# Kernel tuning notes

Hardware: AMD Instinct MI355X
Metric: run time of the kernel (lower is better)

The kernel has to match this reference:

```python
import jax, jax.numpy as jnp
import numpy as np

D = 768      # embed_dim
L = 8        # depth
NH = 4       # num_heads
HD = D // NH # head_dim = 192
GS = 16      # grid size (max_grid_size)
S = GS * GS  # 256 tokens
B = 64
EPS = 1.1920929e-07  # torch.finfo(float32).eps (RMSNorm eps=None)


def rmsnorm(x):
    return x * jax.lax.rsqrt(jnp.mean(x * x, axis=-1, keepdims=True) + EPS)


def householder_Q(vs):
    # sequential chain of Householder reflections: Q <- Q - (2/||v||^2) v (v^T Q)
    def step(Q, v):
        v = v[:, None]
        Q = Q - (2.0 / (jnp.sum(v * v) + 1e-08)) * (v @ (v.T @ Q))
        return Q, None
    Q, _ = jax.lax.scan(step, jnp.eye(vs.shape[1], dtype=vs.dtype), vs)
    return Q


def setup_inputs() -> dict:
    key = jax.random.key(0)
    ks = jax.random.split(key, 16)
    r = lambda k, shape, s=0.02: jax.random.normal(k, shape, jnp.float32) * s
    return dict(
        z_t=jax.random.normal(ks[0], (B, 3, 32, 32), jnp.float32),
        logsnr=jax.random.normal(ks[1], (B,), jnp.float32),
        qkv_w=r(ks[2], (L, D, 3 * D)),
        out_w=r(ks[3], (L, D, D)),
        gate_w=r(ks[4], (L, D, D)), gate_b=jnp.zeros((L, D), jnp.float32),
        mlpg_w=r(ks[5], (L, D, 8 * D)), mlpg_b=jnp.zeros((L, 8 * D), jnp.float32),
        mlpo_w=r(ks[6], (L, 4 * D, D)), mlpo_b=jnp.zeros((L, D), jnp.float32),
        hh_vs=r(ks[7], (L, HD // 2, HD)),
        patch_w=r(ks[8], (20, D)), patch_b=jnp.zeros((D,), jnp.float32),
        head_w=r(ks[9], (D, 12)), head_b=jnp.zeros((12,), jnp.float32),
        sd1_w=r(ks[10], (8, D)), sd1_b=jnp.zeros((D,), jnp.float32),
        sd2_w=r(ks[11], (D, 12)), sd2_b=jnp.zeros((12,), jnp.float32),
        lam_w=r(ks[12], (D, 1)), lam_b=jnp.zeros((1,), jnp.float32),
    )


def reference(z_t, logsnr, qkv_w, out_w, gate_w, gate_b, mlpg_w, mlpg_b,
              mlpo_w, mlpo_b, hh_vs, patch_w, patch_b, head_w, head_b,
              sd1_w, sd1_b, sd2_w, sd2_b, lam_w, lam_b):
    Bn, C, Him, Wim = z_t.shape
    gh = Him // 2
    # patchify 2x2 -> [B, S, 12]
    patches = z_t.reshape(Bn, C, gh, 2, gh, 2).transpose(0, 2, 4, 1, 3, 5).reshape(Bn, S, 12)
    # FourierFeatures(num_bands=4) -> 8-dim sin/cos embedding of logsnr
    bands = 2.0 ** jnp.arange(4, dtype=jnp.float32)
    ang = logsnr[:, None] * bands
    spins = jnp.concatenate([jnp.sin(ang), jnp.cos(ang)], axis=-1)  # [B, 8]
    x = jnp.concatenate([patches, jnp.broadcast_to(spins[:, None, :], (Bn, S, 8))], axis=-1) @ patch_w + patch_b

    # 2D RoPE tables on the 16x16 grid
    yy, xx = jnp.meshgrid(jnp.arange(GS), jnp.arange(GS), indexing='ij')
    coords = jnp.stack([yy.ravel(), xx.ravel()], axis=1).astype(jnp.float32)  # [S, 2]
    dim_half = HD // 2
    inv_freq = 1.0 / 10000.0 ** (jnp.arange(0, dim_half, 2, dtype=jnp.float32) / dim_half)
    fy = coords[:, 0:1] * inv_freq
    fx = coords[:, 1:2] * inv_freq
    emb = jnp.concatenate([fy, fx, fy, fx], axis=-1)  # [S, HD]
    cos, sin = jnp.cos(emb), jnp.sin(emb)

    # local sliding-window mask: euclidean distance on grid < 2.5
    d2 = jnp.sum((coords[:, None, :] - coords[None, :, :]) ** 2, axis=-1)
    local_mask = d2 < 2.5 ** 2  # [S, S]
    is_glob = jnp.array([(i + 1) % 4 == 0 for i in range(L)])
    scale = 1.0 / jnp.sqrt(jnp.float32(HD))

    def layer(x, p):
        qw, ow, gw, gb, mgw, mgb, mow, mob, vs, glob = p
        h = rmsnorm(x)
        q, k, v = jnp.split(h @ qw, 3, axis=-1)
        heads = lambda t: t.reshape(Bn, S, NH, HD).transpose(0, 2, 1, 3)  # [B,H,S,hd]
        q, k, v = heads(q), heads(k), heads(v)
        # RnRoPE: inverse Householder -> rotate -> forward Householder
        Q = householder_Q(vs)
        q, k = q @ Q.T, k @ Q.T
        def rot(t):
            t1, t2 = jnp.split(t, 2, axis=-1)
            return t * cos + jnp.concatenate([-t2, t1], axis=-1) * sin
        q, k = rot(q) @ Q, rot(k) @ Q
        scores = jnp.einsum('bhqd,bhkd->bhqk', q, k) * scale
        keep = local_mask | glob  # global layers attend everywhere
        scores = jnp.where(keep, scores, -1e30)
        attn = jax.nn.softmax(scores, axis=-1) @ v  # [B,H,S,hd]
        attn = attn.transpose(0, 2, 1, 3).reshape(Bn, S, D) @ ow
        gate = jax.nn.sigmoid(attn @ gw + gb)
        x = x + attn * gate
        g, val = jnp.split(rmsnorm(x) @ mgw + mgb, 2, axis=-1)
        x = x + (val * jax.nn.gelu(g, approximate=False)) @ mow + mob
        return x, None

    x, _ = jax.lax.scan(layer, x, (qkv_w, out_w, gate_w, gate_b, mlpg_w, mlpg_b,
                                   mlpo_w, mlpo_b, hh_vs, is_glob))
    x = rmsnorm(x)
    z_pred = x @ head_w + head_b  # [B, S, 12]
    # factorized mode: FourierScaleDecoder scale and lambda head
    scale_f = jnp.exp(jax.nn.silu(spins @ sd1_w + sd1_b) @ sd2_w + sd2_b)  # [B, 12]
    z_pred = z_pred * scale_f[:, None, :]
    l_pred = (jnp.mean(x, axis=1) @ lam_w + lam_b)[:, 0]
    z_img = z_pred.reshape(Bn, gh, gh, 3, 2, 2).transpose(0, 3, 1, 4, 2, 5).reshape(Bn, C, Him, Wim)
    return z_img, l_pred
```

## Files before the change

### kernel.cpp

```cpp
#include <hip/hip_runtime.h>
#include <hip/hip_bf16.h>
#include <math.h>


#define DEV static __device__ __forceinline__

typedef float    f32x4 __attribute__((ext_vector_type(4)));
typedef short    s16x8 __attribute__((ext_vector_type(8)));
typedef unsigned short u16x8 __attribute__((ext_vector_type(8)));
typedef unsigned short u16x4 __attribute__((ext_vector_type(4)));

constexpr int Bb = 64, Ss = 256, Dd = 768, Ll = 8, NHh = 4, HDd = 192;
constexpr int M_TOK = Bb * Ss;
constexpr float EPS_RMS = 1.1920929e-07f;
constexpr float ATT_SCALE = 0.07216878364870322f;
constexpr size_t ARENA_K = (size_t)Bb * NHh * Ss * HDd;

constexpr size_t B_SPINS  = 0;
constexpr size_t B_SCALEF = 2048;
constexpr size_t B_QT     = 5120;
constexpr size_t B_COS    = B_QT + 1179648;
constexpr size_t B_SIN    = B_COS + 196608;
constexpr size_t B_G      = B_SIN + 196608;
constexpr size_t B_T      = B_G + 294912;
constexpr size_t B_AWY    = B_T + 294912;
constexpr size_t B_ROWLAM = B_AWY + 589824;
constexpr size_t B_X      = B_ROWLAM + 65536;
constexpr size_t B_H      = B_X + 50331648;
constexpr size_t B_PROJ   = B_H + 25165824;
constexpr size_t B_WEFFT  = B_PROJ + 25165824;
constexpr size_t B_OUTWT  = B_WEFFT + 28311552;
constexpr size_t B_GATEWT = B_OUTWT + 9437184;
constexpr size_t B_MLPGT  = B_GATEWT + 9437184;
constexpr size_t B_MLPOT  = B_MLPGT + 75497472;
constexpr size_t B_ARENA  = B_MLPOT + 37748736;

DEV float sigmoidf_(float x) { return 1.0f / (1.0f + expf(-x)); }
DEV float geluf_(float g)    { return 0.5f * g * (1.0f + erff(g * 0.7071067811865476f)); }
DEV unsigned short f2bf(float f) {
    union { float f; unsigned u; } a; a.f = f;
    unsigned u = a.u + 0x7fffu + ((a.u >> 16) & 1u);
    return (unsigned short)(u >> 16);
}
DEV float b2f(unsigned short u) {
    union { unsigned u; float f; } a; a.u = ((unsigned)u) << 16; return a.f;
}
DEV void gload16(const void* g, void* l) {
    __builtin_amdgcn_global_load_lds((const __attribute__((address_space(1))) void*)g,
                                     (__attribute__((address_space(3))) void*)l, 16, 0, 0);
}

DEV void xcd_chunk(int gx, int gy, int CX, int& bx, int& by) {
    int id = by * gx + bx;
    int c = id & 7;
    int s = id >> 3;
    int CY = gy >> 3;
    int subsz = CY * CX;
    int bxc = s / subsz;
    int r = s - bxc * subsz;
    int byl = r / CX;
    by = c * CY + byl;
    bx = bxc * CX + (r - byl * CX);
}

__global__ void spins_kernel(const float* __restrict__ logsnr, float* __restrict__ spins) {
    int b = threadIdx.x;
    if (b < 64) {
        float v = logsnr[b];
#pragma unroll
        for (int j = 0; j < 4; ++j) {
            float ang = v * (float)(1 << j);
            spins[b * 8 + j]     = sinf(ang);
            spins[b * 8 + 4 + j] = cosf(ang);
        }
    }
}

__global__ void rope_table_kernel(float* __restrict__ cosb, float* __restrict__ sinb) {
    int s = blockIdx.x, j = threadIdx.x;
    int y = s >> 4, x = s & 15;
    int base = j % 96;
    float coord, invf;
    if (base < 48) { invf = expf(-(float)base * (2.0f / 96.0f) * 9.210340371976184f); coord = (float)y; }
    else { int i = base - 48; invf = expf(-(float)i * (2.0f / 96.0f) * 9.210340371976184f); coord = (float)x; }
    float f = coord * invf, sv, cv;
    sincosf(f, &sv, &cv);
    cosb[s * 192 + j] = cv;
    sinb[s * 192 + j] = sv;
}

__global__ __launch_bounds__(256) void hh_gram_kernel(const float* __restrict__ hh_vs,
                                                      float* __restrict__ Gm) {
    __shared__ float Y[96][192];
    int l = blockIdx.x, t = threadIdx.x;
    const float4* src = (const float4*)(hh_vs + (size_t)l * 96 * 192);
    for (int i = t; i < 4608; i += 256) ((float4*)&Y[0][0])[i] = src[i];
    __syncthreads();
    for (int e = t; e < 9216; e += 256) {
        int i = e / 96, j = e - (e / 96) * 96;
        float acc = 0.f;
        for (int d = 0; d < 48; ++d) {
            float4 a = *(const float4*)&Y[i][d * 4];
            float4 b = *(const float4*)&Y[j][d * 4];
            acc += a.x * b.x + a.y * b.y + a.z * b.z + a.w * b.w;
        }
        Gm[(size_t)l * 9216 + e] = acc;
    }
}

__global__ __launch_bounds__(128) void hh_t_kernel(const float* __restrict__ Gm,
                                                   float* __restrict__ Tm) {
    __shared__ float G[96][96];
    __shared__ float Tt[96][96];
    int l = blockIdx.x, t = threadIdx.x;
    const float* Gl = Gm + (size_t)l * 9216;
    for (int i = t; i < 9216; i += 128) { ((float*)G)[i] = Gl[i]; ((float*)Tt)[i] = 0.f; }
    __syncthreads();
    if (t < 96) Tt[t][t] = 2.0f / (G[t][t] + 1e-8f);
    __syncthreads();
    for (int j = 1; j < 96; ++j) {
        if (t < 96) {
            float cj = 2.0f / (G[j][j] + 1e-8f);
            float dot = 0.f;
            for (int p = 0; p < j; ++p) dot += Tt[p][t] * G[p][j];
            if (t < j) Tt[j][t] = -cj * dot;
        }
        __syncthreads();
    }
    for (int i = t; i < 9216; i += 128) Tm[(size_t)l * 9216 + i] = ((float*)Tt)[i];
}

__global__ __launch_bounds__(256) void hh_a_kernel(const float* __restrict__ Tm,
                                                   const float* __restrict__ hh_vs,
                                                   float* __restrict__ Am) {
    __shared__ float T[96][96];
    __shared__ float Y[96][192];
    int l = blockIdx.x, t = threadIdx.x;
    const float* Tl = Tm + (size_t)l * 9216;
    const float4* src = (const float4*)(hh_vs + (size_t)l * 96 * 192);
    for (int i = t; i < 9216; i += 256) ((float*)T)[i] = Tl[i];
    for (int i = t; i < 4608; i += 256) ((float4*)&Y[0][0])[i] = src[i];
    __syncthreads();
    for (int idx = t; idx < 4608; idx += 256) {
        int i = idx / 48, e0 = (idx % 48) * 4;
        float4 acc = {0.f, 0.f, 0.f, 0.f};
        for (int j = i; j < 96; ++j) {
            float tv = T[j][i];
            float4 y = *(const float4*)&Y[j][e0];
            acc.x += tv * y.x; acc.y += tv * y.y; acc.z += tv * y.z; acc.w += tv * y.w;
        }
        *(float4*)(Am + (size_t)l * 96 * 192 + (size_t)i * 192 + e0) = acc;
    }
}

__global__ __launch_bounds__(256) void hh_p_kernel(const float* __restrict__ hh_vs,
                                                   const float* __restrict__ Am,
                                                   float* __restrict__ qt) {
    __shared__ float Y[96][192];
    __shared__ float A[96][192];
    int l = blockIdx.x, t = threadIdx.x;
    const float4* ys = (const float4*)(hh_vs + (size_t)l * 96 * 192);
    const float4* as = (const float4*)(Am + (size_t)l * 96 * 192);
    for (int i = t; i < 4608; i += 256) { ((float4*)&Y[0][0])[i] = ys[i]; ((float4*)&A[0][0])[i] = as[i]; }
    __syncthreads();
    for (int idx = t; idx < 9216; idx += 256) {
        int d = idx / 48, e0 = (idx % 48) * 4;
        float4 acc = {0.f, 0.f, 0.f, 0.f};
        for (int i = 0; i < 96; ++i) {
            float yv = Y[i][d];
            float4 a = *(const float4*)&A[i][e0];
            acc.x += yv * a.x; acc.y += yv * a.y; acc.z += yv * a.z; acc.w += yv * a.w;
        }
        acc.x = (d == e0 + 0 ? 1.f : 0.f) - acc.x;
        acc.y = (d == e0 + 1 ? 1.f : 0.f) - acc.y;
        acc.z = (d == e0 + 2 ? 1.f : 0.f) - acc.z;
        acc.w = (d == e0 + 3 ? 1.f : 0.f) - acc.w;
        *(float4*)(qt + (size_t)l * 192 * 192 + (size_t)d * 192 + e0) = acc;
    }
}

__global__ __launch_bounds__(256) void fold_bf16t(const float* __restrict__ qkv_w,
                                                  const float* __restrict__ qt,
                                                  unsigned short* __restrict__ weff_t) {
    int z = blockIdx.z;
    int l = z >> 3, which = (z >> 2) & 1, head = z & 3;
    const float* A  = qkv_w + (size_t)l * 768 * 2304 + (size_t)which * 768 + head * 192;
    const float* Bq = qt + (size_t)l * 192 * 192;
    unsigned short* C = weff_t + (size_t)l * 2304 * 768 + ((size_t)which * 768 + head * 192) * 768;
    int row0 = blockIdx.y * 64, col0 = blockIdx.x * 64;
    __shared__ float As[64][65];
    __shared__ float Bs[64][65];
    int tid = threadIdx.x, tx = tid & 15, ty = tid >> 4;
    float acc[4][4] = {};
    for (int k0 = 0; k0 < 192; k0 += 64) {
        for (int i = tid; i < 1024; i += 256) {
            int r = i >> 4, kq = i & 15;
            float4 va = *(const float4*)(A + (size_t)(row0 + r) * 2304 + k0 + kq * 4);
            As[kq * 4 + 0][r] = va.x; As[kq * 4 + 1][r] = va.y; As[kq * 4 + 2][r] = va.z; As[kq * 4 + 3][r] = va.w;
        }
        for (int i = tid; i < 1024; i += 256) {
            int r = i >> 4, nq = i & 15;
            float4 vb = *(const float4*)(Bq + (size_t)(k0 + r) * 192 + col0 + nq * 4);
            Bs[r][nq * 4 + 0] = vb.x; Bs[r][nq * 4 + 1] = vb.y; Bs[r][nq * 4 + 2] = vb.z; Bs[r][nq * 4 + 3] = vb.w;
        }
        __syncthreads();
        for (int k = 0; k < 64; ++k) {
            float a[4], bb[4];
#pragma unroll
            for (int m = 0; m < 4; ++m) a[m] = As[k][ty * 4 + m];
#pragma unroll
            for (int n = 0; n < 4; ++n) bb[n] = Bs[k][tx * 4 + n];
#pragma unroll
            for (int m = 0; m < 4; ++m)
#pragma unroll
                for (int n = 0; n < 4; ++n) acc[m][n] = fmaf(a[m], bb[n], acc[m][n]);
        }
        __syncthreads();
    }
    float (*Tr)[65] = (float(*)[65])As;
#pragma unroll
    for (int m = 0; m < 4; ++m)
#pragma unroll
        for (int n = 0; n < 4; ++n) Tr[tx * 4 + n][ty * 4 + m] = acc[m][n];
    __syncthreads();
    int nl = tid >> 2, kc = (tid & 3) * 16;
#pragma unroll
    for (int q4 = 0; q4 < 4; ++q4) {
        u16x4 o;
#pragma unroll
        for (int ii = 0; ii < 4; ++ii) o[ii] = f2bf(Tr[nl][kc + q4 * 4 + ii]);
        *(u16x4*)(C + (size_t)(col0 + nl) * 768 + row0 + kc + q4 * 4) = o;
    }
}

__global__ __launch_bounds__(256) void transpose_bf16_kernel(const float* __restrict__ W,
                                                             int ldw, size_t zsrc,
                                                             unsigned short* __restrict__ Wt,
                                                             int ldwt, size_t zdst) {
    __shared__ float t[32][33];
    const float* Wz = W + (size_t)blockIdx.z * zsrc;
    unsigned short* Wtz = Wt + (size_t)blockIdx.z * zdst;
    int k0 = blockIdx.y * 32, n0 = blockIdx.x * 32;
    int tid = threadIdx.x;
    int tr = tid >> 3, tc = tid & 7;
    float4 v = *(const float4*)(Wz + (size_t)(k0 + tr) * ldw + n0 + tc * 4);
    t[tr][tc * 4 + 0] = v.x; t[tr][tc * 4 + 1] = v.y; t[tr][tc * 4 + 2] = v.z; t[tr][tc * 4 + 3] = v.w;
    __syncthreads();
    u16x4 o;
    o[0] = f2bf(t[tc * 4 + 0][tr]); o[1] = f2bf(t[tc * 4 + 1][tr]);
    o[2] = f2bf(t[tc * 4 + 2][tr]); o[3] = f2bf(t[tc * 4 + 3][tr]);
    *(u16x4*)(Wtz + (size_t)(n0 + tr) * ldwt + k0 + tc * 4) = o;
}

__global__ __launch_bounds__(256) void patch_embed_kernel(const float* __restrict__ z_t,
                                                          const float* __restrict__ spins,
                                                          const float* __restrict__ patch_w,
                                                          const float* __restrict__ patch_b,
                                                          float* __restrict__ x) {
    int bs = blockIdx.x;
    int b = bs >> 8, s = bs & 255;
    int gy = s >> 4, gx = s & 15;
    __shared__ float in20[20];
    int t = threadIdx.x;
    if (t < 12) {
        int c = t >> 2, py = (t >> 1) & 1, px = t & 1;
        in20[t] = z_t[(((size_t)b * 3 + c) * 32 + (2 * gy + py)) * 32 + (2 * gx + px)];
    } else if (t < 20) {
        in20[t] = spins[b * 8 + (t - 12)];
    }
    __syncthreads();
    for (int d = t; d < 768; d += 256) {
        float acc = patch_b[d];
#pragma unroll
        for (int i = 0; i < 20; ++i) acc += in20[i] * patch_w[i * 768 + d];
        x[(size_t)bs * 768 + d] = acc;
    }
}

__global__ __launch_bounds__(256) void rmsnorm_kernel(const float* __restrict__ x,
                                                      unsigned short* __restrict__ h) {
    int wave = threadIdx.x >> 6, lane = threadIdx.x & 63;
    int row = blockIdx.x * 4 + wave;
    const float* xr = x + (size_t)row * 768 + lane * 12;
    float4 a = *(const float4*)(xr);
    float4 b = *(const float4*)(xr + 4);
    float4 c = *(const float4*)(xr + 8);
    float ss = a.x*a.x + a.y*a.y + a.z*a.z + a.w*a.w
             + b.x*b.x + b.y*b.y + b.z*b.z + b.w*b.w
             + c.x*c.x + c.y*c.y + c.z*c.z + c.w*c.w;
#pragma unroll
    for (int msk = 1; msk < 64; msk <<= 1) ss += __shfl_xor(ss, msk);
    float sc = 1.0f / sqrtf(ss / 768.0f + EPS_RMS);
    unsigned short* hr = h + (size_t)row * 768 + lane * 12;
    u16x4 o0, o1, o2;
    o0[0]=f2bf(a.x*sc); o0[1]=f2bf(a.y*sc); o0[2]=f2bf(a.z*sc); o0[3]=f2bf(a.w*sc);
    o1[0]=f2bf(b.x*sc); o1[1]=f2bf(b.y*sc); o1[2]=f2bf(b.z*sc); o1[3]=f2bf(b.w*sc);
    o2[0]=f2bf(c.x*sc); o2[1]=f2bf(c.y*sc); o2[2]=f2bf(c.z*sc); o2[3]=f2bf(c.w*sc);
    *(u16x4*)(hr) = o0; *(u16x4*)(hr + 4) = o1; *(u16x4*)(hr + 8) = o2;
}

template <int EPI>
__global__ __launch_bounds__(256) void gemm_mfma(const unsigned short* __restrict__ A, int lda,
                                                 const unsigned short* __restrict__ Bt, int ldb,
                                                 unsigned short* __restrict__ Cb, int ldc, int K,
                                                 const float* __restrict__ bias,
                                                 float* __restrict__ Xf,
                                                 const unsigned short* __restrict__ Pb,
                                                 int CX) {
    __shared__ unsigned short As[2][4096];
    __shared__ unsigned short Bs[2][4096];
    int tid = threadIdx.x;
    int wave = tid >> 6, lane = tid & 63;
    int bx = blockIdx.x, by = blockIdx.y;
    xcd_chunk(gridDim.x, gridDim.y, CX, bx, by);
    int row0 = by * 128, col0 = bx * 128;
    int wm = wave >> 1, wn = wave & 1;
    f32x4 acc[4][4] = {};

    int srow = lane >> 2;
    int ksw = (((lane & 3) ^ (srow & 3)) * 8);
    int lrow = lane & 15;
    int csw = (((lane >> 4) ^ (lane & 3)) * 8);

    auto stage = [&](int buf, int k0) {
#pragma unroll
        for (int it = 0; it < 2; ++it) {
            int chunk = it * 4 + wave;
            int r = chunk * 16 + srow;
            gload16(A  + (size_t)(row0 + r) * lda + k0 + ksw, &As[buf][chunk * 512]);
            gload16(Bt + (size_t)(col0 + r) * ldb + k0 + ksw, &Bs[buf][chunk * 512]);
        }
    };

    int NT = K >> 5;
    stage(0, 0);
    for (int t = 0; t < NT; ++t) {
        if (t + 1 < NT) {
            stage((t + 1) & 1, (t + 1) << 5);
            asm volatile("s_waitcnt vmcnt(4)" ::: "memory");
        } else {
            asm volatile("s_waitcnt vmcnt(0)" ::: "memory");
        }
        __builtin_amdgcn_s_barrier();
        const unsigned short* Ab = As[t & 1];
        const unsigned short* Bb = Bs[t & 1];
        s16x8 af[4], bf[4];
#pragma unroll
        for (int m = 0; m < 4; ++m)
            af[m] = *(const s16x8*)&Ab[(wm * 64 + m * 16 + lrow) * 32 + csw];
#pragma unroll
        for (int n = 0; n < 4; ++n)
            bf[n] = *(const s16x8*)&Bb[(wn * 64 + n * 16 + lrow) * 32 + csw];
#pragma unroll
        for (int m = 0; m < 4; ++m)
#pragma unroll
            for (int n = 0; n < 4; ++n)
                acc[m][n] = __builtin_amdgcn_mfma_f32_16x16x32_bf16(af[m], bf[n], acc[m][n], 0, 0, 0);
        __builtin_amdgcn_s_barrier();
    }

    int lquad = lane >> 4;
#pragma unroll
    for (int m = 0; m < 4; ++m) {
#pragma unroll
        for (int n = 0; n < 4; ++n) {
#pragma unroll
            for (int r = 0; r < 4; ++r) {
                int i = row0 + wm * 64 + m * 16 + lquad * 4 + r;
                int j = col0 + wn * 64 + n * 16 + lrow;
                float v = acc[m][n][r];
                if (bias) v += bias[j];
                if constexpr (EPI == 0) {
                    Cb[(size_t)i * ldc + j] = f2bf(v);
                } else if constexpr (EPI == 1) {
                    int which = j / 768;
                    int rem = j - which * 768;
                    int head = rem / 192;
                    int hd = rem - head * 192;
                    int b = i >> 8, s = i & 255;
                    if (which == 2) {
                        Cb[2 * ARENA_K + (((size_t)(b * 4 + head)) * 192 + hd) * 256 + s] = f2bf(v);
                    } else {
                        Cb[(size_t)which * ARENA_K + (((size_t)(b * 4 + head)) * 256 + s) * 192 + hd] = f2bf(v);
                    }
                } else if constexpr (EPI == 2) {
                    float p = b2f(Pb[(size_t)i * 768 + j]);
                    Xf[(size_t)i * 768 + j] += p * sigmoidf_(v);
                } else if constexpr (EPI == 4) {
                    Xf[(size_t)i * ldc + j] += v;
                }
            }
        }
    }
}

__global__ __launch_bounds__(512) void gemm_mlp_fused(const unsigned short* __restrict__ A,
                                                      const unsigned short* __restrict__ Bt,
                                                      unsigned short* __restrict__ Hid,
                                                      const float* __restrict__ bias,
                                                      int CX) {
    __shared__ unsigned short As[8192];
    __shared__ unsigned short Bs[8192];
    int tid = threadIdx.x;
    int wave = tid >> 6, lane = tid & 63;
    int bx = blockIdx.x, by = blockIdx.y;
    xcd_chunk(gridDim.x, gridDim.y, CX, bx, by);
    int row0 = by * 256, col0 = bx * 64;
    int wm = wave >> 1, wn = wave & 1;
    f32x4 accg[4][2] = {};
    f32x4 accv[4][2] = {};

    int srow = lane >> 2;
    int ksw = (((lane & 3) ^ (srow & 3)) * 8);
    int lrow = lane & 15;
    int csw = (((lane >> 4) ^ (lane & 3)) * 8);

    const unsigned short* Bg = Bt + (size_t)col0 * 768;
    const unsigned short* Bv = Bt + (size_t)(3072 + col0) * 768;

    for (int k0 = 0; k0 < 768; k0 += 32) {
#pragma unroll
        for (int it = 0; it < 2; ++it) {
            int chunk = it * 8 + wave;
            int r = chunk * 16 + srow;
            gload16(A + (size_t)(row0 + r) * 768 + k0 + ksw, &As[chunk * 512]);
        }
        {
            int half = wave >> 2;
            int chunk = wave & 3;
            int r = chunk * 16 + srow;
            const unsigned short* Bh = half ? Bv : Bg;
            gload16(Bh + (size_t)r * 768 + k0 + ksw, &Bs[half * 4096 + chunk * 512]);
        }
        __syncthreads();
        s16x8 af[4], bgf[2], bvf[2];
#pragma unroll
        for (int m = 0; m < 4; ++m)
            af[m] = *(const s16x8*)&As[(wm * 64 + m * 16 + lrow) * 32 + csw];
#pragma unroll
        for (int n = 0; n < 2; ++n) {
            bgf[n] = *(const s16x8*)&Bs[(wn * 32 + n * 16 + lrow) * 32 + csw];
            bvf[n] = *(const s16x8*)&Bs[4096 + (wn * 32 + n * 16 + lrow) * 32 + csw];
        }
#pragma unroll
        for (int m = 0; m < 4; ++m)
#pragma unroll
            for (int n = 0; n < 2; ++n) {
                accg[m][n] = __builtin_amdgcn_mfma_f32_16x16x32_bf16(af[m], bgf[n], accg[m][n], 0, 0, 0);
                accv[m][n] = __builtin_amdgcn_mfma_f32_16x16x32_bf16(af[m], bvf[n], accv[m][n], 0, 0, 0);
            }
        __syncthreads();
    }

    int lquad = lane >> 4;
#pragma unroll
    for (int m = 0; m < 4; ++m) {
#pragma unroll
        for (int n = 0; n < 2; ++n) {
#pragma unroll
            for (int r = 0; r < 4; ++r) {
                int i = row0 + wm * 64 + m * 16 + lquad * 4 + r;
                int j = col0 + wn * 32 + n * 16 + lrow;
                float g = accg[m][n][r] + bias[j];
                float v = accv[m][n][r] + bias[3072 + j];
                Hid[(size_t)i * 3072 + j] = f2bf(v * geluf_(g));
            }
        }
    }
}

__global__ __launch_bounds__(512) void attn_mfma_kernel(const unsigned short* __restrict__ qb_,
                                                        const unsigned short* __restrict__ kb_,
                                                        const unsigned short* __restrict__ vtb_,
                                                        unsigned short* __restrict__ attnb,
                                                        const float* __restrict__ cosb,
                                                        const float* __restrict__ sinb,
                                                        int glob) {
    __shared__ unsigned short Klds[256 * 200];
    __shared__ unsigned short Vlds[192 * 72];
    __shared__ unsigned short Plds[8 * 16 * 72];
    int b = blockIdx.z, hh = blockIdx.y;
    int tid = threadIdx.x;
    int wave = tid >> 6, lane = tid & 63;
    int q0 = blockIdx.x * 128 + wave * 16;
    int yq = q0 >> 4;
    size_t bh = (size_t)(b * 4 + hh);
    const unsigned short* qb  = qb_  + bh * 49152;
    const unsigned short* kb  = kb_  + bh * 49152;
    const unsigned short* vtb = vtb_ + bh * 49152;

    for (int c = tid; c < 6144; c += 512) {
        int r = c / 24, col = c - (c / 24) * 24;
        int j0 = col * 8;
        int jp = j0 < 96 ? j0 + 96 : j0 - 96;
        float sgn = j0 < 96 ? -1.f : 1.f;
        u16x8 a = *(const u16x8*)(kb + (size_t)r * 192 + j0);
        u16x8 p = *(const u16x8*)(kb + (size_t)r * 192 + jp);
        const float* cr = cosb + r * 192 + j0;
        const float* sr = sinb + r * 192 + j0;
        u16x8 o;
#pragma unroll
        for (int i = 0; i < 8; ++i)
            o[i] = f2bf(b2f(a[i]) * cr[i] + sgn * b2f(p[i]) * sr[i]);
        *(u16x8*)&Klds[r * 200 + j0] = o;
    }
    __syncthreads();

    s16x8 qf[6];
    {
        int sq = q0 + (lane & 15);
        const unsigned short* qrow = qb + (size_t)sq * 192;
        const float* cr = cosb + sq * 192;
        const float* sr = sinb + sq * 192;
#pragma unroll
        for (int kk = 0; kk < 6; ++kk) {
            int ck = kk * 32 + (lane >> 4) * 8;
            int cp = ck < 96 ? ck + 96 : ck - 96;
            float sgn = ck < 96 ? -1.f : 1.f;
            u16x8 a = *(const u16x8*)(qrow + ck);
            u16x8 p = *(const u16x8*)(qrow + cp);
            s16x8 o;
#pragma unroll
            for (int i = 0; i < 8; ++i)
                o[i] = (short)f2bf(b2f(a[i]) * cr[ck + i] + sgn * b2f(p[i]) * sr[ck + i]);
            qf[kk] = o;
        }
    }

    f32x4 sc[16];
#pragma unroll
    for (int n = 0; n < 16; ++n) sc[n] = (f32x4){0.f, 0.f, 0.f, 0.f};
#pragma unroll
    for (int kk = 0; kk < 6; ++kk) {
#pragma unroll
        for (int n = 0; n < 16; ++n) {
            if (glob || (n >= yq - 2 && n <= yq + 2)) {
                s16x8 bf = *(const s16x8*)&Klds[(n * 16 + (lane & 15)) * 200 + kk * 32 + (lane >> 4) * 8];
                sc[n] = __builtin_amdgcn_mfma_f32_16x16x32_bf16(qf[kk], bf, sc[n], 0, 0, 0);
            }
        }
    }

    int lq = (lane >> 4) * 4;
#pragma unroll
    for (int n = 0; n < 16; ++n) {
        int sk = n * 16 + (lane & 15);
        int yk = sk >> 4, xk = sk & 15;
#pragma unroll
        for (int r = 0; r < 4; ++r) {
            int sq = q0 + lq + r;
            int dy = (sq >> 4) - yk, dx = (sq & 15) - xk;
            bool keep = glob || (dy * dy + dx * dx) < 7;
            sc[n][r] = keep ? sc[n][r] * ATT_SCALE : -1e30f;
        }
    }
    float rmax[4], rsum[4];
#pragma unroll
    for (int r = 0; r < 4; ++r) {
        float m = sc[0][r];
#pragma unroll
        for (int n = 1; n < 16; ++n) m = fmaxf(m, sc[n][r]);
#pragma unroll
        for (int msk = 1; msk < 16; msk <<= 1) m = fmaxf(m, __shfl_xor(m, msk));
        rmax[r] = m;
    }
#pragma unroll
    for (int r = 0; r < 4; ++r) {
        float e = 0.f;
#pragma unroll
        for (int n = 0; n < 16; ++n) { float p = expf(sc[n][r] - rmax[r]); sc[n][r] = p; e += p; }
#pragma unroll
        for (int msk = 1; msk < 16; msk <<= 1) e += __shfl_xor(e, msk);
        rsum[r] = 1.0f / e;
    }

    f32x4 o[12];
#pragma unroll
    for (int n = 0; n < 12; ++n) o[n] = (f32x4){0.f, 0.f, 0.f, 0.f};
    unsigned short* Pw = &Plds[wave * 1152];
    int ylo = blockIdx.x * 8 - 2, yhi = blockIdx.x * 8 + 9;
    for (int kt = 0; kt < 4; ++kt) {
        if (!glob && !((4 * kt + 3 >= ylo) && (4 * kt <= yhi))) continue;
#pragma unroll
        for (int nn = 0; nn < 4; ++nn) {
#pragma unroll
            for (int r = 0; r < 4; ++r)
                Pw[(lq + r) * 72 + nn * 16 + (lane & 15)] = f2bf(sc[kt * 4 + nn][r] * rsum[r]);
        }
        __syncthreads();
        for (int c = tid; c < 1536; c += 512) {
            int r = c >> 3, col = c & 7;
            *(u16x8*)&Vlds[r * 72 + col * 8] = *(const u16x8*)(vtb + (size_t)r * 256 + kt * 64 + col * 8);
        }
        __syncthreads();
        s16x8 af[2];
#pragma unroll
        for (int kk2 = 0; kk2 < 2; ++kk2)
            af[kk2] = *(const s16x8*)&Pw[(lane & 15) * 72 + kk2 * 32 + (lane >> 4) * 8];
#pragma unroll
        for (int n = 0; n < 12; ++n) {
#pragma unroll
            for (int kk2 = 0; kk2 < 2; ++kk2) {
                s16x8 bf = *(const s16x8*)&Vlds[(n * 16 + (lane & 15)) * 72 + kk2 * 32 + (lane >> 4) * 8];
                o[n] = __builtin_amdgcn_mfma_f32_16x16x32_bf16(af[kk2], bf, o[n], 0, 0, 0);
            }
        }
    }
#pragma unroll
    for (int n = 0; n < 12; ++n) {
        int d = n * 16 + (lane & 15);
#pragma unroll
        for (int r = 0; r < 4; ++r) {
            int sq = q0 + lq + r;
            attnb[((size_t)(b * 256 + sq)) * 768 + hh * 192 + d] = f2bf(o[n][r]);
        }
    }
}

__global__ __launch_bounds__(768) void scalef_kernel(const float* __restrict__ spins,
                                                     const float* __restrict__ sd1_w,
                                                     const float* __restrict__ sd1_b,
                                                     const float* __restrict__ sd2_w,
                                                     const float* __restrict__ sd2_b,
                                                     float* __restrict__ scalef) {
    int b = blockIdx.x, t = threadIdx.x;
    __shared__ float hid[768];
    __shared__ float sp[8];
    if (t < 8) sp[t] = spins[b * 8 + t];
    __syncthreads();
    float acc = sd1_b[t];
#pragma unroll
    for (int i = 0; i < 8; ++i) acc += sp[i] * sd1_w[i * 768 + t];
    hid[t] = acc * sigmoidf_(acc);
    __syncthreads();
    if (t < 12) {
        float o = sd2_b[t];
        for (int d = 0; d < 768; ++d) o += hid[d] * sd2_w[d * 12 + t];
        scalef[b * 12 + t] = expf(o);
    }
}

__global__ __launch_bounds__(256) void head_kernel(const unsigned short* __restrict__ xn,
                                                   const float* __restrict__ head_w,
                                                   const float* __restrict__ head_b,
                                                   const float* __restrict__ scalef,
                                                   const float* __restrict__ lam_w,
                                                   float* __restrict__ out,
                                                   float* __restrict__ rowlam) {
    __shared__ float hw[768][13];
    __shared__ float red[4][64][14];
    int t = threadIdx.x, wave = t >> 6, lane = t & 63;
    for (int i = t; i < 768 * 12; i += 256) hw[i / 12][i % 12] = head_w[i];
    for (int i = t; i < 768; i += 256) hw[i][12] = lam_w[i];
    __syncthreads();
    int row_base = blockIdx.x * 64;
    for (int rr = wave; rr < 64; rr += 4) {
        int row = row_base + rr;
        const unsigned short* xr = xn + (size_t)row * 768 + lane * 12;
        float xv[12];
        u16x4 v0 = *(const u16x4*)(xr);
        u16x4 v1 = *(const u16x4*)(xr + 4);
        u16x4 v2 = *(const u16x4*)(xr + 8);
#pragma unroll
        for (int j = 0; j < 4; ++j) { xv[j] = b2f(v0[j]); xv[4 + j] = b2f(v1[j]); xv[8 + j] = b2f(v2[j]); }
        float p[13] = {};
        int d0 = lane * 12;
#pragma unroll
        for (int dd = 0; dd < 12; ++dd) {
            float xvv = xv[dd];
#pragma unroll
            for (int o = 0; o < 12; ++o) p[o] += xvv * hw[d0 + dd][o];
            p[12] += xvv * hw[d0 + dd][12];
        }
#pragma unroll
        for (int o = 0; o < 13; ++o) red[wave][lane][o] = p[o];
        __syncthreads();
        if (lane < 13) {
            float s = 0.f;
            for (int i = 0; i < 64; ++i) s += red[wave][i][lane];
            if (lane < 12) {
                int b = row >> 8, sidx = row & 255;
                float v = (s + head_b[lane]) * scalef[b * 12 + lane];
                int c = lane >> 2, py = (lane >> 1) & 1, px = lane & 1;
                int gy = sidx >> 4, gxx = sidx & 15;
                out[(((size_t)b * 3 + c) * 32 + 2 * gy + py) * 32 + 2 * gxx + px] = v;
            } else {
                rowlam[row] = s;
            }
        }
        __syncthreads();
    }
}

__global__ __launch_bounds__(256) void lpred_kernel(const float* __restrict__ rowlam,
                                                    const float* __restrict__ lam_b,
                                                    float* __restrict__ out) {
    int b = blockIdx.x, t = threadIdx.x;
    __shared__ float red[256];
    red[t] = rowlam[b * 256 + t];
    __syncthreads();
    for (int s2 = 128; s2 > 0; s2 >>= 1) { if (t < s2) red[t] += red[t + s2]; __syncthreads(); }
    if (t == 0) out[196608 + b] = red[0] / 256.0f + lam_b[0];
}

extern "C" void kernel_launch(void* const* d_in, const int* in_sizes, int n_in,
                              void* d_out, int out_size, void* d_ws, size_t ws_size,
                              hipStream_t stream) {
    const float* z_t     = (const float*)d_in[0];
    const float* logsnr  = (const float*)d_in[1];
    const float* qkv_w   = (const float*)d_in[2];
    const float* out_w   = (const float*)d_in[3];
    const float* gate_w  = (const float*)d_in[4];
    const float* gate_b  = (const float*)d_in[5];
    const float* mlpg_w  = (const float*)d_in[6];
    const float* mlpg_b  = (const float*)d_in[7];
    const float* mlpo_w  = (const float*)d_in[8];
    const float* mlpo_b  = (const float*)d_in[9];
    const float* hh_vs   = (const float*)d_in[10];
    const float* patch_w = (const float*)d_in[11];
    const float* patch_b = (const float*)d_in[12];
    const float* head_w  = (const float*)d_in[13];
    const float* head_b  = (const float*)d_in[14];
    const float* sd1_w   = (const float*)d_in[15];
    const float* sd1_b   = (const float*)d_in[16];
    const float* sd2_w   = (const float*)d_in[17];
    const float* sd2_b   = (const float*)d_in[18];
    const float* lam_w   = (const float*)d_in[19];
    const float* lam_b   = (const float*)d_in[20];

    char* wsb = (char*)d_ws;
    float* spins  = (float*)(wsb + B_SPINS);
    float* scalef = (float*)(wsb + B_SCALEF);
    float* qt     = (float*)(wsb + B_QT);
    float* cosb   = (float*)(wsb + B_COS);
    float* sinb   = (float*)(wsb + B_SIN);
    float* Gm     = (float*)(wsb + B_G);
    float* Tm     = (float*)(wsb + B_T);
    float* Am     = (float*)(wsb + B_AWY);
    float* rowlam = (float*)(wsb + B_ROWLAM);
    float* x      = (float*)(wsb + B_X);
    unsigned short* h      = (unsigned short*)(wsb + B_H);
    unsigned short* proj   = (unsigned short*)(wsb + B_PROJ);
    unsigned short* weff_t = (unsigned short*)(wsb + B_WEFFT);
    unsigned short* outw_t = (unsigned short*)(wsb + B_OUTWT);
    unsigned short* gatew_t= (unsigned short*)(wsb + B_GATEWT);
    unsigned short* mlpg_t = (unsigned short*)(wsb + B_MLPGT);
    unsigned short* mlpo_t = (unsigned short*)(wsb + B_MLPOT);
    unsigned short* arena  = (unsigned short*)(wsb + B_ARENA);
    unsigned short* qbuf = arena;
    unsigned short* kbuf = arena + ARENA_K;
    unsigned short* vtbuf = arena + 2 * ARENA_K;
    unsigned short* attnb = arena + 3 * ARENA_K;
    unsigned short* hidden = arena;
    float* out = (float*)d_out;

    spins_kernel<<<1, 64, 0, stream>>>(logsnr, spins);
    rope_table_kernel<<<256, 192, 0, stream>>>(cosb, sinb);
    hh_gram_kernel<<<8, 256, 0, stream>>>(hh_vs, Gm);
    hh_t_kernel<<<8, 128, 0, stream>>>(Gm, Tm);
    hh_a_kernel<<<8, 256, 0, stream>>>(Tm, hh_vs, Am);
    hh_p_kernel<<<8, 256, 0, stream>>>(hh_vs, Am, qt);
    fold_bf16t<<<dim3(3, 12, 64), 256, 0, stream>>>(qkv_w, qt, weff_t);
    transpose_bf16_kernel<<<dim3(24, 24, 8), 256, 0, stream>>>(qkv_w + 1536, 2304,
        (size_t)768 * 2304, weff_t + (size_t)1536 * 768, 768, (size_t)2304 * 768);
    transpose_bf16_kernel<<<dim3(24, 24, 8), 256, 0, stream>>>(out_w, 768,
        (size_t)768 * 768, outw_t, 768, (size_t)768 * 768);
    transpose_bf16_kernel<<<dim3(24, 24, 8), 256, 0, stream>>>(gate_w, 768,
        (size_t)768 * 768, gatew_t, 768, (size_t)768 * 768);
    transpose_bf16_kernel<<<dim3(192, 24, 8), 256, 0, stream>>>(mlpg_w, 6144,
        (size_t)768 * 6144, mlpg_t, 768, (size_t)6144 * 768);
    transpose_bf16_kernel<<<dim3(24, 96, 8), 256, 0, stream>>>(mlpo_w, 768,
        (size_t)3072 * 768, mlpo_t, 3072, (size_t)768 * 3072);
    patch_embed_kernel<<<M_TOK, 256, 0, stream>>>(z_t, spins, patch_w, patch_b, x);

    for (int l = 0; l < Ll; ++l) {
        int glob = ((l + 1) % 4 == 0) ? 1 : 0;
        rmsnorm_kernel<<<4096, 256, 0, stream>>>(x, h);
        gemm_mfma<1><<<dim3(18, 128), 256, 0, stream>>>(h, 768,
            weff_t + (size_t)l * 2304 * 768, 768, arena, 0, 768, nullptr, nullptr, nullptr, 3);
        attn_mfma_kernel<<<dim3(2, 4, 64), 512, 0, stream>>>(qbuf, kbuf, vtbuf, attnb,
            cosb, sinb, glob);
        gemm_mfma<0><<<dim3(6, 128), 256, 0, stream>>>(attnb, 768,
            outw_t + (size_t)l * 768 * 768, 768, proj, 768, 768, nullptr, nullptr, nullptr, 3);
        gemm_mfma<2><<<dim3(6, 128), 256, 0, stream>>>(proj, 768,
            gatew_t + (size_t)l * 768 * 768, 768, nullptr, 768, 768,
            gate_b + (size_t)l * 768, x, proj, 3);
        rmsnorm_kernel<<<4096, 256, 0, stream>>>(x, h);
        gemm_mlp_fused<<<dim3(48, 64), 512, 0, stream>>>(h,
            mlpg_t + (size_t)l * 6144 * 768, hidden, mlpg_b + (size_t)l * 6144, 4);
        gemm_mfma<4><<<dim3(6, 128), 256, 0, stream>>>(hidden, 3072,
            mlpo_t + (size_t)l * 768 * 3072, 3072, nullptr, 768, 3072,
            mlpo_b + (size_t)l * 768, x, nullptr, 6);
    }

    rmsnorm_kernel<<<4096, 256, 0, stream>>>(x, h);
    scalef_kernel<<<64, 768, 0, stream>>>(spins, sd1_w, sd1_b, sd2_w, sd2_b, scalef);
    head_kernel<<<256, 256, 0, stream>>>(h, head_w, head_b, scalef, lam_w, out, rowlam);
    lpred_kernel<<<64, 256, 0, stream>>>(rowlam, lam_b, out);
}
```

Before: 5.548 ms.

## Fuse out-proj and gate GEMMs via precomputed out_w@gate_w product

Precomputes W2 = out_w·gate_w per layer in bf16, then computes attn@out_w and attn@W2 in one fused kernel that applies the sigmoid gate residual directly. This removes the intermediate proj buffer round-trip and one dependent GEMM launch per layer. It adds an fp32 SIMT weight-product kernel at setup and changes rounding slightly.

```diff
diff --git a/kernel.cpp b/kernel.cpp
--- a/kernel.cpp
+++ b/kernel.cpp
@@ -33,7 +33,8 @@
 constexpr size_t B_GATEWT = B_OUTWT + 9437184;
 constexpr size_t B_MLPGT  = B_GATEWT + 9437184;
 constexpr size_t B_MLPOT  = B_MLPGT + 75497472;
-constexpr size_t B_ARENA  = B_MLPOT + 37748736;
+constexpr size_t B_W2T    = B_MLPOT + 37748736;
+constexpr size_t B_ARENA  = B_W2T + 9437184;
 
 DEV float sigmoidf_(float x) { return 1.0f / (1.0f + expf(-x)); }
 DEV float geluf_(float g)    { return 0.5f * g * (1.0f + erff(g * 0.7071067811865476f)); }
@@ -233,6 +234,59 @@
     }
 }
 
+__global__ __launch_bounds__(256) void w2_bf16t(const float* __restrict__ ow,
+                                                const float* __restrict__ gw,
+                                                unsigned short* __restrict__ w2t) {
+    int l = blockIdx.z;
+    const float* A = ow + (size_t)l * 768 * 768;
+    const float* B = gw + (size_t)l * 768 * 768;
+    unsigned short* C = w2t + (size_t)l * 768 * 768;
+    int row0 = blockIdx.y * 64, col0 = blockIdx.x * 64;
+    __shared__ float As[64][65];
+    __shared__ float Bs[64][65];
+    int tid = threadIdx.x, tx = tid & 15, ty = tid >> 4;
+    float acc[4][4] = {};
+    for (int k0 = 0; k0 < 768; k0 += 64) {
+        for (int i = tid; i < 1024; i += 256) {
+            int r = i >> 4, kq = i & 15;
+            float4 va = *(const float4*)(A + (size_t)(row0 + r) * 768 + k0 + kq * 4);
+            As[kq * 4 + 0][r] = va.x; As[kq * 4 + 1][r] = va.y; As[kq * 4 + 2][r] = va.z; As[kq * 4 + 3][r] = va.w;
+        }
+        for (int i = tid; i < 1024; i += 256) {
+            int r = i >> 4, nq = i & 15;
+            float4 vb = *(const float4*)(B + (size_t)(k0 + r) * 768 + col0 + nq * 4);
+            Bs[r][nq * 4 + 0] = vb.x; Bs[r][nq * 4 + 1] = vb.y; Bs[r][nq * 4 + 2] = vb.z; Bs[r][nq * 4 + 3] = vb.w;
+        }
+        __syncthreads();
+        for (int k = 0; k < 64; ++k) {
+            float a[4], bb[4];
+#pragma unroll
+            for (int m = 0; m < 4; ++m) a[m] = As[k][ty * 4 + m];
+#pragma unroll
+            for (int n = 0; n < 4; ++n) bb[n] = Bs[k][tx * 4 + n];
+#pragma unroll
+            for (int m = 0; m < 4; ++m)
+#pragma unroll
+                for (int n = 0; n < 4; ++n) acc[m][n] = fmaf(a[m], bb[n], acc[m][n]);
+        }
+        __syncthreads();
+    }
+    float (*Tr)[65] = (float(*)[65])As;
+#pragma unroll
+    for (int m = 0; m < 4; ++m)
+#pragma unroll
+        for (int n = 0; n < 4; ++n) Tr[tx * 4 + n][ty * 4 + m] = acc[m][n];
+    __syncthreads();
+    int nl = tid >> 2, kc = (tid & 3) * 16;
+#pragma unroll
+    for (int q4 = 0; q4 < 4; ++q4) {
+        u16x4 o;
+#pragma unroll
+        for (int ii = 0; ii < 4; ++ii) o[ii] = f2bf(Tr[nl][kc + q4 * 4 + ii]);
+        *(u16x4*)(C + (size_t)(col0 + nl) * 768 + row0 + kc + q4 * 4) = o;
+    }
+}
+
 __global__ __launch_bounds__(256) void transpose_bf16_kernel(const float* __restrict__ W,
                                                              int ldw, size_t zsrc,
                                                              unsigned short* __restrict__ Wt,
@@ -370,9 +424,7 @@
                 int j = col0 + wn * 64 + n * 16 + lrow;
                 float v = acc[m][n][r];
                 if (bias) v += bias[j];
-                if constexpr (EPI == 0) {
-                    Cb[(size_t)i * ldc + j] = f2bf(v);
-                } else if constexpr (EPI == 1) {
+                if constexpr (EPI == 1) {
                     int which = j / 768;
                     int rem = j - which * 768;
                     int head = rem / 192;
@@ -383,9 +435,6 @@
                     } else {
                         Cb[(size_t)which * ARENA_K + (((size_t)(b * 4 + head)) * 256 + s) * 192 + hd] = f2bf(v);
                     }
-                } else if constexpr (EPI == 2) {
-                    float p = b2f(Pb[(size_t)i * 768 + j]);
-                    Xf[(size_t)i * 768 + j] += p * sigmoidf_(v);
                 } else if constexpr (EPI == 4) {
                     Xf[(size_t)i * ldc + j] += v;
                 }
@@ -464,6 +513,82 @@
                 float g = accg[m][n][r] + bias[j];
                 float v = accv[m][n][r] + bias[3072 + j];
                 Hid[(size_t)i * 3072 + j] = f2bf(v * geluf_(g));
+            }
+        }
+    }
+}
+
+__global__ __launch_bounds__(512) void gemm_projgate(const unsigned short* __restrict__ A,
+                                                     const unsigned short* __restrict__ B1t,
+                                                     const unsigned short* __restrict__ B2t,
+                                                     const float* __restrict__ gate_b,
+                                                     float* __restrict__ Xf,
+                                                     int CX) {
+    __shared__ unsigned short As[8192];
+    __shared__ unsigned short Bs[8192];
+    int tid = threadIdx.x;
+    int wave = tid >> 6, lane = tid & 63;
+    int bx = blockIdx.x, by = blockIdx.y;
+    xcd_chunk(gridDim.x, gridDim.y, CX, bx, by);
+    int row0 = by * 256, col0 = bx * 64;
+    int wm = wave >> 1, wn = wave & 1;
+    f32x4 accp[4][2] = {};
+    f32x4 accg[4][2] = {};
+
+    int srow = lane >> 2;
+    int ksw = (((lane & 3) ^ (srow & 3)) * 8);
+    int lrow = lane & 15;
+    int csw = (((lane >> 4) ^ (lane & 3)) * 8);
+
+    const unsigned short* B1 = B1t + (size_t)col0 * 768;
+    const unsigned short* B2 = B2t + (size_t)col0 * 768;
+
+    for (int k0 = 0; k0 < 768; k0 += 32) {
+#pragma unroll
+        for (int it = 0; it < 2; ++it) {
+            int chunk = it * 8 + wave;
+            int r = chunk * 16 + srow;
+            gload16(A + (size_t)(row0 + r) * 768 + k0 + ksw, &As[chunk * 512]);
+        }
+        {
+            int half = wave >> 2;
+            int chunk = wave & 3;
+            int r = chunk * 16 + srow;
+            const unsigned short* Bh = half ? B2 : B1;
+            gload16(Bh + (size_t)r * 768 + k0 + ksw, &Bs[half * 4096 + chunk * 512]);
+        }
+        __syncthreads();
+        s16x8 af[4], b1f[2], b2f_[2];
+#pragma unroll
+        for (int m = 0; m < 4; ++m)
+            af[m] = *(const s16x8*)&As[(wm * 64 + m * 16 + lrow) * 32 + csw];
+#pragma unroll
+        for (int n = 0; n < 2; ++n) {
+            b1f[n]  = *(const s16x8*)&Bs[(wn * 32 + n * 16 + lrow) * 32 + csw];
+            b2f_[n] = *(const s16x8*)&Bs[4096 + (wn * 32 + n * 16 + lrow) * 32 + csw];
+        }
+#pragma unroll
+        for (int m = 0; m < 4; ++m)
+#pragma unroll
+            for (int n = 0; n < 2; ++n) {
+                accp[m][n] = __builtin_amdgcn_mfma_f32_16x16x32_bf16(af[m], b1f[n],  accp[m][n], 0, 0, 0);
+                accg[m][n] = __builtin_amdgcn_mfma_f32_16x16x32_bf16(af[m], b2f_[n], accg[m][n], 0, 0, 0);
+            }
+        __syncthreads();
+    }
+
+    int lquad = lane >> 4;
+#pragma unroll
+    for (int m = 0; m < 4; ++m) {
+#pragma unroll
+        for (int n = 0; n < 2; ++n) {
+#pragma unroll
+            for (int r = 0; r < 4; ++r) {
+                int i = row0 + wm * 64 + m * 16 + lquad * 4 + r;
+                int j = col0 + wn * 32 + n * 16 + lrow;
+                float p1 = accp[m][n][r];
+                float p2 = accg[m][n][r] + gate_b[j];
+                Xf[(size_t)i * 768 + j] += p1 * sigmoidf_(p2);
             }
         }
     }
@@ -740,12 +865,11 @@
     float* rowlam = (float*)(wsb + B_ROWLAM);
     float* x      = (float*)(wsb + B_X);
     unsigned short* h      = (unsigned short*)(wsb + B_H);
-    unsigned short* proj   = (unsigned short*)(wsb + B_PROJ);
     unsigned short* weff_t = (unsigned short*)(wsb + B_WEFFT);
     unsigned short* outw_t = (unsigned short*)(wsb + B_OUTWT);
-    unsigned short* gatew_t= (unsigned short*)(wsb + B_GATEWT);
     unsigned short* mlpg_t = (unsigned short*)(wsb + B_MLPGT);
     unsigned short* mlpo_t = (unsigned short*)(wsb + B_MLPOT);
+    unsigned short* w2_t   = (unsigned short*)(wsb + B_W2T);
     unsigned short* arena  = (unsigned short*)(wsb + B_ARENA);
     unsigned short* qbuf = arena;
     unsigned short* kbuf = arena + ARENA_K;
@@ -765,8 +889,7 @@
         (size_t)768 * 2304, weff_t + (size_t)1536 * 768, 768, (size_t)2304 * 768);
     transpose_bf16_kernel<<<dim3(24, 24, 8), 256, 0, stream>>>(out_w, 768,
         (size_t)768 * 768, outw_t, 768, (size_t)768 * 768);
-    transpose_bf16_kernel<<<dim3(24, 24, 8), 256, 0, stream>>>(gate_w, 768,
-        (size_t)768 * 768, gatew_t, 768, (size_t)768 * 768);
+    w2_bf16t<<<dim3(12, 12, 8), 256, 0, stream>>>(out_w, gate_w, w2_t);
     transpose_bf16_kernel<<<dim3(192, 24, 8), 256, 0, stream>>>(mlpg_w, 6144,
         (size_t)768 * 6144, mlpg_t, 768, (size_t)6144 * 768);
     transpose_bf16_kernel<<<dim3(24, 96, 8), 256, 0, stream>>>(mlpo_w, 768,
@@ -780,11 +903,9 @@
             weff_t + (size_t)l * 2304 * 768, 768, arena, 0, 768, nullptr, nullptr, nullptr, 3);
         attn_mfma_kernel<<<dim3(2, 4, 64), 512, 0, stream>>>(qbuf, kbuf, vtbuf, attnb,
             cosb, sinb, glob);
-        gemm_mfma<0><<<dim3(6, 128), 256, 0, stream>>>(attnb, 768,
-            outw_t + (size_t)l * 768 * 768, 768, proj, 768, 768, nullptr, nullptr, nullptr, 3);
-        gemm_mfma<2><<<dim3(6, 128), 256, 0, stream>>>(proj, 768,
-            gatew_t + (size_t)l * 768 * 768, 768, nullptr, 768, 768,
-            gate_b + (size_t)l * 768, x, proj, 3);
+        gemm_projgate<<<dim3(12, 64), 512, 0, stream>>>(attnb,
+            outw_t + (size_t)l * 768 * 768, w2_t + (size_t)l * 768 * 768,
+            gate_b + (size_t)l * 768, x, 3);
         rmsnorm_kernel<<<4096, 256, 0, stream>>>(x, h);
         gemm_mlp_fused<<<dim3(48, 64), 512, 0, stream>>>(h,
             mlpg_t + (size_t)l * 6144 * 768, hidden, mlpg_b + (size_t)l * 6144, 4);
```

Measured after the change: 5.483 ms. About the same (-1.2%).
